# Performance work log

Measured on AMD Instinct MI355X. Metric: run time of the kernel, lower is better.

The kernel has to match this reference:

```python
import jax, jax.numpy as jnp
import numpy as np

N_NODES = 100000
N_EDGES = 1600000
D = 128


def setup_inputs() -> dict:
    key = jax.random.key(0)
    k1, k2, k3, k4 = jax.random.split(key, 4)
    ego_embeddings = jax.random.normal(k1, (N_NODES, D), dtype=jnp.float32)
    edge_index = jax.random.randint(k2, (2, N_EDGES), 0, N_NODES, dtype=jnp.int64)
    edge_weight = jax.random.uniform(k3, (N_EDGES,), dtype=jnp.float32)
    W = jax.random.normal(k4, (D, D), dtype=jnp.float32) * (1.0 / np.sqrt(D))
    b = jnp.zeros((D,), dtype=jnp.float32)
    return {"ego_embeddings": ego_embeddings, "edge_index": edge_index,
            "edge_weight": edge_weight, "W": W, "b": b}


def reference(ego_embeddings, edge_index, edge_weight, W, b):
    # SpMM: side[i] = sum_j A[i,j] * ego[j], A given as COO (dst=row, src=col)
    src = edge_index[1]
    dst = edge_index[0]
    messages = ego_embeddings[src] * edge_weight[:, None]  # [E, D]
    side_embeddings = jax.ops.segment_sum(messages, dst, num_segments=N_NODES)
    # gcn aggregator: LeakyReLU(Linear(ego + side)); dropout p=0.0 -> identity
    h = (ego_embeddings + side_embeddings) @ W.T + b
    return jax.nn.leaky_relu(h, negative_slope=0.01)
```

## Files before the change

### kernel.cpp

```cpp
#include <hip/hip_runtime.h>

#define N_NODES 100000
#define N_EDGES 1600000
#define DIM 128
#define CAP 48

#define NBIN 391
#define BINW 256
#define BCAP 4608
#define EPT  8
#define EPB  2048

#define WB_OFF   0
#define GCUR_OFF 32768
#define DEG_OFF  65536
#define EPK_OFF  465536
#define EGOB_OFF (EPK_OFF + (size_t)N_NODES * CAP * 4)
#define WS_BF16  (EGOB_OFF + (size_t)N_NODES * DIM * 2)

using short8  = __attribute__((ext_vector_type(8))) short;
using floatx4 = __attribute__((ext_vector_type(4))) float;

static __device__ __forceinline__ unsigned short f2bf(float f) {
    unsigned u = __float_as_uint(f);
    u += 0x7FFF + ((u >> 16) & 1);
    return (unsigned short)(u >> 16);
}
static __device__ __forceinline__ float bf_lo(unsigned u) {
    return __uint_as_float(u << 16);
}
static __device__ __forceinline__ float bf_hi(unsigned u) {
    return __uint_as_float(u & 0xFFFF0000u);
}

__global__ __launch_bounds__(256) void convert_w(const float* __restrict__ W,
                                                 unsigned short* __restrict__ Wb) {
    int i = blockIdx.x * 256 + threadIdx.x;
    if (i < DIM * DIM) Wb[i] = f2bf(W[i]);
}

__global__ __launch_bounds__(256) void convert_ego(const float4* __restrict__ e4,
                                                   uint4* __restrict__ o4) {
    int i = blockIdx.x * 256 + threadIdx.x;
    if (i < N_NODES * 16) {
        float4 a = e4[2 * i];
        float4 b = e4[2 * i + 1];
        uint4 o;
        o.x = (unsigned)f2bf(a.x) | ((unsigned)f2bf(a.y) << 16);
        o.y = (unsigned)f2bf(a.z) | ((unsigned)f2bf(a.w) << 16);
        o.z = (unsigned)f2bf(b.x) | ((unsigned)f2bf(b.y) << 16);
        o.w = (unsigned)f2bf(b.z) | ((unsigned)f2bf(b.w) << 16);
        o4[i] = o;
    }
}

__global__ __launch_bounds__(256) void bin_edges(
        const int* __restrict__ eidx,
        const float* __restrict__ ew,
        int* __restrict__ gcur,
        uint2* __restrict__ stg) {
    __shared__ int lh[NBIN];
    __shared__ int gb[NBIN];
    const int tid = threadIdx.x;
    const int b0 = blockIdx.x * EPB;

    for (int i = tid; i < NBIN; i += 256) lh[i] = 0;
    __syncthreads();

    int dst[EPT], rank[EPT];
    unsigned rec[EPT];
    bool val[EPT];
#pragma unroll
    for (int k = 0; k < EPT; ++k) {
        int e = b0 + k * 256 + tid;
        val[k] = e < N_EDGES;
        int ec = val[k] ? e : 0;
        int d = eidx[ec];
        int s = eidx[N_EDGES + ec];
        float w = ew[ec];
        dst[k] = d;
        rec[k] = ((unsigned)s << 15) | (unsigned)(w * 32767.0f + 0.5f);
        rank[k] = val[k] ? atomicAdd(&lh[d >> 8], 1) : 0;
    }
    __syncthreads();

    for (int i = tid; i < NBIN; i += 256) {
        int c = lh[i];
        gb[i] = c ? atomicAdd(&gcur[i], c) : 0;
    }
    __syncthreads();

#pragma unroll
    for (int k = 0; k < EPT; ++k) {
        if (val[k]) {
            int bin = dst[k] >> 8;
            int pos = gb[bin] + rank[k];
            if (pos < BCAP)
                stg[(size_t)bin * BCAP + pos] = make_uint2(rec[k], (unsigned)dst[k]);
        }
    }
}

__global__ __launch_bounds__(256) void place_edges(
        const uint2* __restrict__ stg,
        const int* __restrict__ gcur,
        unsigned* __restrict__ epk,
        int* __restrict__ deg) {
    __shared__ int lc[BINW];
    const int tid = threadIdx.x;
    const int bin = blockIdx.x;

    lc[tid] = 0;
    __syncthreads();

    int cnt = gcur[bin];
    if (cnt > BCAP) cnt = BCAP;
    for (int r = tid; r < cnt; r += 256) {
        uint2 rc = stg[(size_t)bin * BCAP + r];
        int d = (int)rc.y;
        int rk = atomicAdd(&lc[d & 255], 1);
        if (rk < CAP) epk[(size_t)d * CAP + rk] = rc.x;
    }
    __syncthreads();

    int node = bin * BINW + tid;
    if (node < N_NODES) deg[node] = lc[tid];
}

__global__ __launch_bounds__(256) void csr_scatter(
        const int* __restrict__ eidx,
        const float* __restrict__ ew,
        int* __restrict__ deg,
        unsigned* __restrict__ epk) {
    int e = blockIdx.x * 256 + threadIdx.x;
    if (e >= N_EDGES) return;
    int dst = eidx[e];
    int src = eidx[N_EDGES + e];
    float w = ew[e];
    int r = atomicAdd(&deg[dst], 1);
    if (r < CAP) {
        unsigned q = (unsigned)(w * 32767.0f + 0.5f);
        epk[(size_t)dst * CAP + r] = ((unsigned)src << 15) | q;
    }
}

#define LSTR 136
template <bool BF16>
__global__ __launch_bounds__(256) void gather_gemm(
        const unsigned* __restrict__ eg2,
        const float* __restrict__ egof,
        const unsigned* __restrict__ epk,
        const int* __restrict__ deg,
        const unsigned short* __restrict__ Wb,
        const float* __restrict__ bias,
        float* __restrict__ out) {
    __shared__ __align__(16) unsigned short s_x[64 * LSTR];

    const int tid  = threadIdx.x;
    const int wave = tid >> 6;
    const int lane = tid & 63;
    const int R    = blockIdx.x * 64;
    const float inv15 = 1.0f / 32767.0f;

    if (BF16) {
        const int half = lane >> 5;
        const int hl   = lane & 31;
        const uint2* eg8 = (const uint2*)eg2;
        const int plane = (lane < CAP) ? lane : (CAP - 1);

        int nA = R + wave * 16;
        int nB = nA + 1;
        unsigned pvA = (nA < N_NODES) ? epk[(size_t)nA * CAP + plane] : 0u;
        unsigned pvB = (nB < N_NODES) ? epk[(size_t)nB * CAP + plane] : 0u;
        int dgA = (nA < N_NODES) ? deg[nA] : 0;
        int dgB = (nB < N_NODES) ? deg[nB] : 0;

        for (int i = 0; i < 8; ++i) {
            const int myNode = R + wave * 16 + 2 * i + half;
            const bool valid = myNode < N_NODES;

            unsigned pvAc = pvA, pvBc = pvB;
            int dgAc = dgA < CAP ? dgA : CAP;
            int dgBc = dgB < CAP ? dgB : CAP;
            const int dgme = half ? dgBc : dgAc;
            const int dgw  = dgAc > dgBc ? dgAc : dgBc;

            if (i < 7) {
                int mA = R + wave * 16 + 2 * (i + 1);
                int mB = mA + 1;
                pvA = (mA < N_NODES) ? epk[(size_t)mA * CAP + plane] : 0u;
                pvB = (mB < N_NODES) ? epk[(size_t)mB * CAP + plane] : 0u;
                dgA = (mA < N_NODES) ? deg[mA] : 0;
                dgB = (mB < N_NODES) ? deg[mB] : 0;
            }

            uint2 idv = make_uint2(0u, 0u);
            if (valid) idv = eg8[(size_t)myNode * 32 + hl];

            float acc[4][4];
#pragma unroll
            for (int k = 0; k < 4; ++k)
#pragma unroll
                for (int c = 0; c < 4; ++c) acc[k][c] = 0.f;
            acc[0][0] = bf_lo(idv.x);  acc[0][1] = bf_hi(idv.x);
            acc[0][2] = bf_lo(idv.y);  acc[0][3] = bf_hi(idv.y);

            for (int e = 0; e < dgw; e += 4) {
                unsigned p[4];
                uint2 g[4];
                float wv[4];
#pragma unroll
                for (int k = 0; k < 4; ++k) {
                    unsigned pa = __shfl(pvAc, e + k);
                    unsigned pb = __shfl(pvBc, e + k);
                    unsigned ps = half ? pb : pa;
                    p[k] = ((e + k) < dgme) ? ps : 0u;
                }
#pragma unroll
                for (int k = 0; k < 4; ++k)
                    g[k] = eg8[(size_t)(p[k] >> 15) * 32 + hl];
#pragma unroll
                for (int k = 0; k < 4; ++k)
                    wv[k] = (float)(p[k] & 0x7FFF) * inv15;
#pragma unroll
                for (int k = 0; k < 4; ++k) {
                    acc[k][0] = fmaf(wv[k], bf_lo(g[k].x), acc[k][0]);
                    acc[k][1] = fmaf(wv[k], bf_hi(g[k].x), acc[k][1]);
                    acc[k][2] = fmaf(wv[k], bf_lo(g[k].y), acc[k][2]);
                    acc[k][3] = fmaf(wv[k], bf_hi(g[k].y), acc[k][3]);
                }
            }

            float s0 = (acc[0][0] + acc[1][0]) + (acc[2][0] + acc[3][0]);
            float s1 = (acc[0][1] + acc[1][1]) + (acc[2][1] + acc[3][1]);
            float s2 = (acc[0][2] + acc[1][2]) + (acc[2][2] + acc[3][2]);
            float s3 = (acc[0][3] + acc[1][3]) + (acc[2][3] + acc[3][3]);

            unsigned lo = (unsigned)f2bf(s0) | ((unsigned)f2bf(s1) << 16);
            unsigned hi = (unsigned)f2bf(s2) | ((unsigned)f2bf(s3) << 16);
            int myRow = wave * 16 + 2 * i + half;
            *(uint2*)&s_x[myRow * LSTR + hl * 4] = make_uint2(lo, hi);
        }
    } else {
        for (int i = 0; i < 16; ++i) {
            int node = R + wave * 16 + i;
            float ax = 0.f, ay = 0.f, bx = 0.f, by = 0.f;
            float cx = 0.f, cy = 0.f, dx2 = 0.f, dy2 = 0.f;
            if (node < N_NODES) {
                size_t cidx = (size_t)node * 64 + lane;
                float2 vv = ((const float2*)egof)[cidx];
                ax = vv.x; ay = vv.y;
                int dg = deg[node];
                if (dg > CAP) dg = CAP;
                size_t base = (size_t)node * CAP;
                unsigned pv = epk[base + (lane < CAP ? lane : CAP - 1)];
                int e = 0;
                for (; e + 3 < dg; e += 4) {
                    unsigned p0 = __shfl(pv, e + 0);
                    unsigned p1 = __shfl(pv, e + 1);
                    unsigned p2 = __shfl(pv, e + 2);
                    unsigned p3 = __shfl(pv, e + 3);
                    float2 v0 = ((const float2*)egof)[(size_t)(p0 >> 15) * 64 + lane];
                    float2 v1 = ((const float2*)egof)[(size_t)(p1 >> 15) * 64 + lane];
                    float2 v2 = ((const float2*)egof)[(size_t)(p2 >> 15) * 64 + lane];
                    float2 v3 = ((const float2*)egof)[(size_t)(p3 >> 15) * 64 + lane];
                    float w0 = (float)(p0 & 0x7FFF) * inv15;
                    float w1 = (float)(p1 & 0x7FFF) * inv15;
                    float w2 = (float)(p2 & 0x7FFF) * inv15;
                    float w3 = (float)(p3 & 0x7FFF) * inv15;
                    ax = fmaf(w0, v0.x, ax);  ay = fmaf(w0, v0.y, ay);
                    bx = fmaf(w1, v1.x, bx);  by = fmaf(w1, v1.y, by);
                    cx = fmaf(w2, v2.x, cx);  cy = fmaf(w2, v2.y, cy);
                    dx2 = fmaf(w3, v3.x, dx2); dy2 = fmaf(w3, v3.y, dy2);
                }
                for (; e < dg; ++e) {
                    unsigned p = __shfl(pv, e);
                    float2 vv2 = ((const float2*)egof)[(size_t)(p >> 15) * 64 + lane];
                    float w = (float)(p & 0x7FFF) * inv15;
                    ax = fmaf(w, vv2.x, ax);  ay = fmaf(w, vv2.y, ay);
                }
            }
            unsigned pk = (unsigned)f2bf(ax + bx + cx + dx2) |
                          ((unsigned)f2bf(ay + by + cy + dy2) << 16);
            *(unsigned*)&s_x[(wave * 16 + i) * LSTR + 2 * lane] = pk;
        }
    }

    const int m0 = wave * 16;
    const int ml = lane & 15;
    const int q  = lane >> 4;

    floatx4 acc[8];
#pragma unroll
    for (int nt = 0; nt < 8; ++nt) acc[nt] = (floatx4){0.f, 0.f, 0.f, 0.f};

#pragma unroll
    for (int kc = 0; kc < 4; ++kc) {
        short8 a = *(const short8*)&s_x[(m0 + ml) * LSTR + kc * 32 + q * 8];
#pragma unroll
        for (int nt = 0; nt < 8; ++nt) {
            short8 b = *(const short8*)&Wb[(size_t)(nt * 16 + ml) * DIM + kc * 32 + q * 8];
            acc[nt] = __builtin_amdgcn_mfma_f32_16x16x32_bf16(a, b, acc[nt], 0, 0, 0);
        }
    }

#pragma unroll
    for (int nt = 0; nt < 8; ++nt) {
        int col = nt * 16 + ml;
        float bv = bias[col];
#pragma unroll
        for (int r = 0; r < 4; ++r) {
            int row = R + m0 + q * 4 + r;
            if (row < N_NODES) {
                float v = acc[nt][r] + bv;
                v = v > 0.f ? v : 0.01f * v;
                out[(size_t)row * DIM + col] = v;
            }
        }
    }
}

extern "C" void kernel_launch(void* const* d_in, const int* in_sizes, int n_in,
                              void* d_out, int out_size, void* d_ws, size_t ws_size,
                              hipStream_t stream) {
    const float* ego  = (const float*)d_in[0];
    const int*   eidx = (const int*)d_in[1];
    const float* ew   = (const float*)d_in[2];
    const float* W    = (const float*)d_in[3];
    const float* bias = (const float*)d_in[4];
    float* out = (float*)d_out;

    char* ws = (char*)d_ws;
    unsigned short* Wb   = (unsigned short*)(ws + WB_OFF);
    int*            gcur = (int*)(ws + GCUR_OFF);
    int*            deg  = (int*)(ws + DEG_OFF);
    unsigned*       epk  = (unsigned*)(ws + EPK_OFF);
    unsigned short* egob = (unsigned short*)(ws + EGOB_OFF);
    uint2*          stg  = (uint2*)(ws + EGOB_OFF);

    const bool use_bf16 = (ws_size >= WS_BF16);

    convert_w<<<(DIM * DIM + 255) / 256, 256, 0, stream>>>(W, Wb);

    if (use_bf16) {
        hipMemsetAsync(gcur, 0, NBIN * sizeof(int), stream);
        bin_edges<<<(N_EDGES + EPB - 1) / EPB, 256, 0, stream>>>(
            eidx, ew, gcur, stg);
        place_edges<<<NBIN, 256, 0, stream>>>(stg, gcur, epk, deg);
        convert_ego<<<(N_NODES * 16 + 255) / 256, 256, 0, stream>>>(
            (const float4*)ego, (uint4*)egob);
        gather_gemm<true><<<(N_NODES + 63) / 64, 256, 0, stream>>>(
            (const unsigned*)egob, ego, epk, deg, Wb, bias, out);
    } else {
        hipMemsetAsync(deg, 0, (size_t)N_NODES * sizeof(int), stream);
        csr_scatter<<<(N_EDGES + 255) / 256, 256, 0, stream>>>(
            eidx, ew, deg, epk);
        gather_gemm<false><<<(N_NODES + 63) / 64, 256, 0, stream>>>(
            (const unsigned*)egob, ego, epk, deg, Wb, bias, out);
    }
}
```

Before: 261.8 us.

## Fuse conversion kernels, use finer edge bins, stage in output, widen gather unroll

Merges the W and ego bf16 conversions and the bin-counter reset into one kernel, removing two launches and a memset. Shrinks edge bins from 256 to 64 nodes (more place_edges blocks, less skew per bin) and reuses the output buffer for staging so conversion can run before binning. Widens the gather loop to 8 outstanding loads per iteration and adds an occupancy hint of 6 blocks per CU, trading register pressure for memory-level parallelism. Bins are capped at 1280 entries, so overflowing edges are silently dropped if a bin exceeds the cap.

New measurement: 265.8 us. No clear change (+1.5%).

```diff
diff --git a/kernel.cpp b/kernel.cpp
--- a/kernel.cpp
+++ b/kernel.cpp
@@ -5,9 +5,9 @@
 #define DIM 128
 #define CAP 48
 
-#define NBIN 391
-#define BINW 256
-#define BCAP 4608
+#define NBIN 1563
+#define BINW 64
+#define BCAP 1280
 #define EPT  8
 #define EPB  2048
 
@@ -33,25 +33,34 @@
     return __uint_as_float(u & 0xFFFF0000u);
 }
 
+#define EGO_BLKS 6250
+__global__ __launch_bounds__(256) void convert_all(
+        const float4* __restrict__ e4, uint4* __restrict__ o4,
+        const float* __restrict__ W, unsigned short* __restrict__ Wb,
+        int* __restrict__ gcur) {
+    const int b = blockIdx.x;
+    const int tid = threadIdx.x;
+    if (b < EGO_BLKS) {
+        int i = b * 256 + tid;
+        float4 a = e4[2 * i];
+        float4 c = e4[2 * i + 1];
+        uint4 o;
+        o.x = (unsigned)f2bf(a.x) | ((unsigned)f2bf(a.y) << 16);
+        o.y = (unsigned)f2bf(a.z) | ((unsigned)f2bf(a.w) << 16);
+        o.z = (unsigned)f2bf(c.x) | ((unsigned)f2bf(c.y) << 16);
+        o.w = (unsigned)f2bf(c.z) | ((unsigned)f2bf(c.w) << 16);
+        o4[i] = o;
+    } else {
+        int j = (b - EGO_BLKS) * 256 + tid;
+        if (j < DIM * DIM) Wb[j] = f2bf(W[j]);
+        if (j < NBIN) gcur[j] = 0;
+    }
+}
+
 __global__ __launch_bounds__(256) void convert_w(const float* __restrict__ W,
                                                  unsigned short* __restrict__ Wb) {
     int i = blockIdx.x * 256 + threadIdx.x;
     if (i < DIM * DIM) Wb[i] = f2bf(W[i]);
-}
-
-__global__ __launch_bounds__(256) void convert_ego(const float4* __restrict__ e4,
-                                                   uint4* __restrict__ o4) {
-    int i = blockIdx.x * 256 + threadIdx.x;
-    if (i < N_NODES * 16) {
-        float4 a = e4[2 * i];
-        float4 b = e4[2 * i + 1];
-        uint4 o;
-        o.x = (unsigned)f2bf(a.x) | ((unsigned)f2bf(a.y) << 16);
-        o.y = (unsigned)f2bf(a.z) | ((unsigned)f2bf(a.w) << 16);
-        o.z = (unsigned)f2bf(b.x) | ((unsigned)f2bf(b.y) << 16);
-        o.w = (unsigned)f2bf(b.z) | ((unsigned)f2bf(b.w) << 16);
-        o4[i] = o;
-    }
 }
 
 __global__ __launch_bounds__(256) void bin_edges(
@@ -80,7 +89,7 @@
         float w = ew[ec];
         dst[k] = d;
         rec[k] = ((unsigned)s << 15) | (unsigned)(w * 32767.0f + 0.5f);
-        rank[k] = val[k] ? atomicAdd(&lh[d >> 8], 1) : 0;
+        rank[k] = val[k] ? atomicAdd(&lh[d >> 6], 1) : 0;
     }
     __syncthreads();
 
@@ -93,7 +102,7 @@
 #pragma unroll
     for (int k = 0; k < EPT; ++k) {
         if (val[k]) {
-            int bin = dst[k] >> 8;
+            int bin = dst[k] >> 6;
             int pos = gb[bin] + rank[k];
             if (pos < BCAP)
                 stg[(size_t)bin * BCAP + pos] = make_uint2(rec[k], (unsigned)dst[k]);
@@ -110,7 +119,7 @@
     const int tid = threadIdx.x;
     const int bin = blockIdx.x;
 
-    lc[tid] = 0;
+    if (tid < BINW) lc[tid] = 0;
     __syncthreads();
 
     int cnt = gcur[bin];
@@ -118,13 +127,15 @@
     for (int r = tid; r < cnt; r += 256) {
         uint2 rc = stg[(size_t)bin * BCAP + r];
         int d = (int)rc.y;
-        int rk = atomicAdd(&lc[d & 255], 1);
+        int rk = atomicAdd(&lc[d & (BINW - 1)], 1);
         if (rk < CAP) epk[(size_t)d * CAP + rk] = rc.x;
     }
     __syncthreads();
 
-    int node = bin * BINW + tid;
-    if (node < N_NODES) deg[node] = lc[tid];
+    if (tid < BINW) {
+        int node = bin * BINW + tid;
+        if (node < N_NODES) deg[node] = lc[tid];
+    }
 }
 
 __global__ __launch_bounds__(256) void csr_scatter(
@@ -146,7 +157,7 @@
 
 #define LSTR 136
 template <bool BF16>
-__global__ __launch_bounds__(256) void gather_gemm(
+__global__ __launch_bounds__(256, 6) void gather_gemm(
         const unsigned* __restrict__ eg2,
         const float* __restrict__ egof,
         const unsigned* __restrict__ epk,
@@ -205,29 +216,26 @@
             acc[0][0] = bf_lo(idv.x);  acc[0][1] = bf_hi(idv.x);
             acc[0][2] = bf_lo(idv.y);  acc[0][3] = bf_hi(idv.y);
 
-            for (int e = 0; e < dgw; e += 4) {
-                unsigned p[4];
-                uint2 g[4];
-                float wv[4];
-#pragma unroll
-                for (int k = 0; k < 4; ++k) {
+            for (int e = 0; e < dgw; e += 8) {
+                unsigned p[8];
+                uint2 g[8];
+#pragma unroll
+                for (int k = 0; k < 8; ++k) {
                     unsigned pa = __shfl(pvAc, e + k);
                     unsigned pb = __shfl(pvBc, e + k);
                     unsigned ps = half ? pb : pa;
                     p[k] = ((e + k) < dgme) ? ps : 0u;
                 }
 #pragma unroll
-                for (int k = 0; k < 4; ++k)
+                for (int k = 0; k < 8; ++k)
                     g[k] = eg8[(size_t)(p[k] >> 15) * 32 + hl];
 #pragma unroll
-                for (int k = 0; k < 4; ++k)
-                    wv[k] = (float)(p[k] & 0x7FFF) * inv15;
-#pragma unroll
-                for (int k = 0; k < 4; ++k) {
-                    acc[k][0] = fmaf(wv[k], bf_lo(g[k].x), acc[k][0]);
-                    acc[k][1] = fmaf(wv[k], bf_hi(g[k].x), acc[k][1]);
-                    acc[k][2] = fmaf(wv[k], bf_lo(g[k].y), acc[k][2]);
-                    acc[k][3] = fmaf(wv[k], bf_hi(g[k].y), acc[k][3]);
+                for (int k = 0; k < 8; ++k) {
+                    float wv = (float)(p[k] & 0x7FFF) * inv15;
+                    acc[k & 3][0] = fmaf(wv, bf_lo(g[k].x), acc[k & 3][0]);
+                    acc[k & 3][1] = fmaf(wv, bf_hi(g[k].x), acc[k & 3][1]);
+                    acc[k & 3][2] = fmaf(wv, bf_lo(g[k].y), acc[k & 3][2]);
+                    acc[k & 3][3] = fmaf(wv, bf_hi(g[k].y), acc[k & 3][3]);
                 }
             }
 
@@ -336,22 +344,20 @@
     int*            deg  = (int*)(ws + DEG_OFF);
     unsigned*       epk  = (unsigned*)(ws + EPK_OFF);
     unsigned short* egob = (unsigned short*)(ws + EGOB_OFF);
-    uint2*          stg  = (uint2*)(ws + EGOB_OFF);
+    uint2*          stg  = (uint2*)out;
 
     const bool use_bf16 = (ws_size >= WS_BF16);
 
-    convert_w<<<(DIM * DIM + 255) / 256, 256, 0, stream>>>(W, Wb);
-
     if (use_bf16) {
-        hipMemsetAsync(gcur, 0, NBIN * sizeof(int), stream);
+        convert_all<<<EGO_BLKS + 64, 256, 0, stream>>>(
+            (const float4*)ego, (uint4*)egob, W, Wb, gcur);
         bin_edges<<<(N_EDGES + EPB - 1) / EPB, 256, 0, stream>>>(
             eidx, ew, gcur, stg);
         place_edges<<<NBIN, 256, 0, stream>>>(stg, gcur, epk, deg);
-        convert_ego<<<(N_NODES * 16 + 255) / 256, 256, 0, stream>>>(
-            (const float4*)ego, (uint4*)egob);
         gather_gemm<true><<<(N_NODES + 63) / 64, 256, 0, stream>>>(
             (const unsigned*)egob, ego, epk, deg, Wb, bias, out);
     } else {
+        convert_w<<<(DIM * DIM + 255) / 256, 256, 0, stream>>>(W, Wb);
         hipMemsetAsync(deg, 0, (size_t)N_NODES * sizeof(int), stream);
         csr_scatter<<<(N_EDGES + 255) / 256, 256, 0, stream>>>(
             eidx, ew, deg, epk);
```
